# Kernel optimization log

Measured on AMD Instinct MI355X. Metric: run time of the kernel, lower is better.

## Reference

```python
import jax, jax.numpy as jnp
import numpy as np

N, E, R = 50000, 1600000, 8
IN_F, HID_F, OUT_F = 128, 64, 64


def setup_inputs() -> dict:
    key = jax.random.key(0)
    ks = jax.random.split(key, 9)
    x = jax.random.normal(ks[0], (N, IN_F), dtype=jnp.float32)
    edge_index = jax.random.randint(ks[1], (2, E), 0, N, dtype=jnp.int64)
    edge_type = jax.random.randint(ks[2], (E,), 0, R, dtype=jnp.int64)
    # layer 1 params (scaled like glorot)
    s1 = 1.0 / np.sqrt(IN_F)
    W1_rel = jax.random.normal(ks[3], (R, IN_F, HID_F), dtype=jnp.float32) * s1
    W1_root = jax.random.normal(ks[4], (IN_F, HID_F), dtype=jnp.float32) * s1
    b1 = jnp.zeros((HID_F,), dtype=jnp.float32)
    # layer 2 params
    s2 = 1.0 / np.sqrt(HID_F)
    W2_rel = jax.random.normal(ks[5], (R, HID_F, OUT_F), dtype=jnp.float32) * s2
    W2_root = jax.random.normal(ks[6], (HID_F, OUT_F), dtype=jnp.float32) * s2
    b2 = jnp.zeros((OUT_F,), dtype=jnp.float32)
    return {"x": x, "edge_index": edge_index, "edge_type": edge_type,
            "W1_rel": W1_rel, "W1_root": W1_root, "b1": b1,
            "W2_rel": W2_rel, "W2_root": W2_root, "b2": b2}


def _rgcn_conv(x, src, dst, etype, W_rel, W_root, b):
    """PyG RGCNConv: root transform + per-relation mean-aggregated messages."""
    n = x.shape[0]
    r = W_rel.shape[0]
    # per-relation transform of all node features: [R, N, H]
    xw = jnp.einsum('nd,rdh->rnh', x, W_rel)
    # per-edge message: transformed source feature under the edge's relation
    msg = xw[etype, src]  # [E, H]
    # mean normalization per (dst, relation) pair
    key = dst * r + etype  # [E]
    cnt = jax.ops.segment_sum(jnp.ones(etype.shape, dtype=x.dtype), key,
                              num_segments=n * r)
    inv = 1.0 / jnp.maximum(cnt, 1.0)
    msg = msg * inv[key][:, None]
    # scatter-add into target nodes
    agg = jax.ops.segment_sum(msg, dst, num_segments=n)  # [N, H]
    return agg + x @ W_root + b


def reference(x, edge_index, edge_type, W1_rel, W1_root, b1, W2_rel, W2_root, b2):
    src, dst = edge_index[0], edge_index[1]
    h = _rgcn_conv(x, src, dst, edge_type, W1_rel, W1_root, b1)
    h = jax.nn.relu(h)
    out = _rgcn_conv(h, src, dst, edge_type, W2_rel, W2_root, b2)
    return out
```

## Files before the change

kernel.cpp:

```cpp
#include <hip/hip_runtime.h>


constexpr int NN  = 50000;
constexpr int NE  = 1600000;
constexpr int NR  = 8;
constexpr int FIN = 128;
constexpr int FH  = 64;

constexpr int BSH = 7;
constexpr int BN  = 1 << BSH;
constexpr int NB  = (NN + BN - 1) >> BSH;
constexpr int CH  = 8192;

typedef __attribute__((ext_vector_type(8))) short bf16x8;
typedef __attribute__((ext_vector_type(4))) float f32x4;

__device__ __forceinline__ unsigned short f2bf(float f) {
  unsigned u = __float_as_uint(f);
  u = (u + 0x7fff + ((u >> 16) & 1)) >> 16;
  return (unsigned short)u;
}
__device__ __forceinline__ float bf2f(unsigned short b) {
  return __uint_as_float(((unsigned)b) << 16);
}
__device__ __forceinline__ bool edge_ok(unsigned s, unsigned d, unsigned r) {
  return s < NN && d < NN && r < NR;
}

__global__ void __launch_bounds__(256) bucket_hist(
    const int* __restrict__ src, const int* __restrict__ dst,
    const int* __restrict__ et, int* __restrict__ bhist) {
  __shared__ int h[NB];
  for (int i = threadIdx.x; i < NB; i += 256) h[i] = 0;
  __syncthreads();
  for (int i = blockIdx.x * 256 + threadIdx.x; i < NE; i += gridDim.x * 256) {
    const unsigned s = (unsigned)src[i];
    const unsigned d = (unsigned)dst[i];
    const unsigned r = (unsigned)et[i];
    if (edge_ok(s, d, r)) atomicAdd(&h[d >> BSH], 1);
  }
  __syncthreads();
  for (int i = threadIdx.x; i < NB; i += 256)
    if (h[i]) atomicAdd(&bhist[i], h[i]);
}

__global__ void __launch_bounds__(256) bucket_prefix(const int* __restrict__ bhist,
                                                     int* __restrict__ bbase,
                                                     int* __restrict__ bcur) {
  __shared__ int wtot[4];
  const int t = threadIdx.x;
  const int v0 = (2 * t < NB) ? bhist[2 * t] : 0;
  const int v1 = (2 * t + 1 < NB) ? bhist[2 * t + 1] : 0;
  const int s  = v0 + v1;
  int incl = s;
#pragma unroll
  for (int o = 1; o < 64; o <<= 1) {
    int u = __shfl_up(incl, o, 64);
    if ((t & 63) >= o) incl += u;
  }
  if ((t & 63) == 63) wtot[t >> 6] = incl;
  __syncthreads();
  int wo = 0;
  for (int w = 0; w < (t >> 6); ++w) wo += wtot[w];
  const int e = wo + incl - s;
  if (2 * t < NB)     { bbase[2 * t] = e;          bcur[2 * t] = e; }
  if (2 * t + 1 < NB) { bbase[2 * t + 1] = e + v0; bcur[2 * t + 1] = e + v0; }
}

__global__ void __launch_bounds__(256) bucket_append(
    const int* __restrict__ src, const int* __restrict__ dst,
    const int* __restrict__ et, int* __restrict__ bcur,
    uint2* __restrict__ brecs) {
  __shared__ uint2 stage[CH];
  __shared__ int h[NB], gbase[NB], sbase[NB], scur[NB];
  __shared__ int wtot[4];
  const int t  = threadIdx.x;
  const int c0 = blockIdx.x * CH;
  const int m  = min(CH, NE - c0);

  for (int i = t; i < NB; i += 256) h[i] = 0;
  __syncthreads();

  for (int i = t; i < m; i += 256) {
    const unsigned s = (unsigned)src[c0 + i];
    const unsigned d = (unsigned)dst[c0 + i];
    const unsigned r = (unsigned)et[c0 + i];
    if (edge_ok(s, d, r)) atomicAdd(&h[d >> BSH], 1);
  }
  __syncthreads();

  const int v0 = (2 * t < NB) ? h[2 * t] : 0;
  const int v1 = (2 * t + 1 < NB) ? h[2 * t + 1] : 0;
  if (2 * t < NB     && v0) gbase[2 * t]     = atomicAdd(&bcur[2 * t], v0);
  if (2 * t + 1 < NB && v1) gbase[2 * t + 1] = atomicAdd(&bcur[2 * t + 1], v1);
  const int s = v0 + v1;
  int incl = s;
#pragma unroll
  for (int o = 1; o < 64; o <<= 1) {
    int u = __shfl_up(incl, o, 64);
    if ((t & 63) >= o) incl += u;
  }
  if ((t & 63) == 63) wtot[t >> 6] = incl;
  __syncthreads();
  int wo = 0;
  for (int w = 0; w < (t >> 6); ++w) wo += wtot[w];
  const int e = wo + incl - s;
  if (2 * t < NB)     { sbase[2 * t] = e;          scur[2 * t] = e; }
  if (2 * t + 1 < NB) { sbase[2 * t + 1] = e + v0; scur[2 * t + 1] = e + v0; }
  __syncthreads();

  for (int i = t; i < m; i += 256) {
    const unsigned sv = (unsigned)src[c0 + i];
    const unsigned d  = (unsigned)dst[c0 + i];
    const unsigned r  = (unsigned)et[c0 + i];
    if (edge_ok(sv, d, r)) {
      const int p = atomicAdd(&scur[d >> BSH], 1);
      stage[p] = make_uint2((sv << 9) | (r << 6), d);
    }
  }
  __syncthreads();

  const int M = sbase[NB - 1] + h[NB - 1];
  for (int j = t; j < M; j += 256) {
    const uint2 rec = stage[j];
    const int b = (int)(rec.y >> BSH);
    brecs[gbase[b] + (j - sbase[b])] = rec;
  }
}

__global__ void __launch_bounds__(256) bucket_finalize(
    const int* __restrict__ bbase, const int* __restrict__ bhist,
    const uint2* __restrict__ brecs, float* __restrict__ inv,
    int* __restrict__ row_start, int* __restrict__ deg,
    unsigned* __restrict__ recs) {
  const int b    = blockIdx.x;
  const int base = bbase[b];
  const int m    = bhist[b];
  const int d0   = b << BSH;
  __shared__ int cnt[BN * NR];
  __shared__ int curs[BN * NR];
  __shared__ int wtot[4];
  const int t = threadIdx.x;

  for (int i = t; i < BN * NR; i += 256) cnt[i] = 0;
  __syncthreads();
  for (int i = t; i < m; i += 256) {
    const uint2 rec = brecs[base + i];
    const int dl = (int)rec.y - d0;
    const int r  = (rec.x >> 6) & 7;
    atomicAdd(&cnt[dl * NR + r], 1);
  }
  __syncthreads();

  const int c0 = cnt[t * 4], c1 = cnt[t * 4 + 1], c2 = cnt[t * 4 + 2], c3 = cnt[t * 4 + 3];
  const int s = c0 + c1 + c2 + c3;
  int incl = s;
#pragma unroll
  for (int o = 1; o < 64; o <<= 1) {
    int u = __shfl_up(incl, o, 64);
    if ((t & 63) >= o) incl += u;
  }
  if ((t & 63) == 63) wtot[t >> 6] = incl;
  __syncthreads();
  int wo = 0;
  for (int w = 0; w < (t >> 6); ++w) wo += wtot[w];
  const int e = wo + incl - s;
  curs[t * 4]     = e;
  curs[t * 4 + 1] = e + c0;
  curs[t * 4 + 2] = e + c0 + c1;
  curs[t * 4 + 3] = e + c0 + c1 + c2;
  __syncthreads();

  if (t < BN) {
    const int d = d0 + t;
    if (d < NN) {
      const int start = curs[t * NR];
      const int end   = (t == BN - 1) ? m : curs[(t + 1) * NR];
      row_start[d] = base + start;
      deg[d]       = end - start;
#pragma unroll
      for (int r = 0; r < NR; ++r)
        inv[d * NR + r] = 1.0f / fmaxf((float)cnt[t * NR + r], 1.0f);
    }
  }
  __syncthreads();

  for (int i = t; i < m; i += 256) {
    const uint2 rec = brecs[base + i];
    const int dl = (int)rec.y - d0;
    const int r  = (rec.x >> 6) & 7;
    const int p  = atomicAdd(&curs[dl * NR + r], 1);
    recs[base + p] = rec.x;
  }
}

template <int K>
__global__ void cvt_w(const float* __restrict__ Wrel, const float* __restrict__ Wroot,
                      unsigned short* __restrict__ Wt) {
  int i = blockIdx.x * blockDim.x + threadIdx.x;
  if (i >= (NR + 1) * 64 * K) return;
  const int g   = i / (64 * K);
  const int rem = i % (64 * K);
  const int n   = rem / K;
  const int k   = rem % K;
  const float* W = (g < NR) ? (Wrel + (size_t)g * K * 64) : Wroot;
  Wt[i] = f2bf(W[k * 64 + n]);
}

template <int K, bool A_FP32>
__global__ void __launch_bounds__(256) gemm_mfma(
    const void* __restrict__ Av, const unsigned short* __restrict__ Wt,
    const float* __restrict__ bias,
    unsigned short* __restrict__ xw, float* __restrict__ root_out) {
  constexpr int KP = K + 8;
  __shared__ unsigned short As[64 * KP];
  __shared__ unsigned short Bs[64 * KP];
  const int n0  = blockIdx.x * 64;
  const int tid = threadIdx.x;

  if constexpr (A_FP32) {
    const float* A = (const float*)Av;
    for (int c = tid; c < 64 * (K / 8); c += 256) {
      const int row = c / (K / 8), kp = (c % (K / 8)) * 8;
      bf16x8 v = {};
      if (n0 + row < NN) {
        const float* p = A + (size_t)(n0 + row) * K + kp;
        const float4 f0 = *(const float4*)p;
        const float4 f1 = *(const float4*)(p + 4);
        v[0] = f2bf(f0.x); v[1] = f2bf(f0.y); v[2] = f2bf(f0.z); v[3] = f2bf(f0.w);
        v[4] = f2bf(f1.x); v[5] = f2bf(f1.y); v[6] = f2bf(f1.z); v[7] = f2bf(f1.w);
      }
      *(bf16x8*)(As + row * KP + kp) = v;
    }
  } else {
    const unsigned short* A = (const unsigned short*)Av;
    for (int c = tid; c < 64 * (K / 8); c += 256) {
      const int row = c / (K / 8), kp = (c % (K / 8)) * 8;
      bf16x8 v = {};
      if (n0 + row < NN) v = *(const bf16x8*)(A + (size_t)(n0 + row) * K + kp);
      *(bf16x8*)(As + row * KP + kp) = v;
    }
  }

  const int wave = tid >> 6, lane = tid & 63;
  const int i16 = lane & 15, quad = lane >> 4;
  const int r0 = wave * 16 + i16;

  for (int g = 0; g <= NR; ++g) {
    __syncthreads();
    const unsigned short* Wg = Wt + (size_t)g * 64 * K;
    for (int c = tid; c < 64 * (K / 8); c += 256) {
      const int row = c / (K / 8), kp = (c % (K / 8)) * 8;
      *(bf16x8*)(Bs + row * KP + kp) = *(const bf16x8*)(Wg + row * K + kp);
    }
    __syncthreads();

    f32x4 acc[4] = {};
#pragma unroll
    for (int kc = 0; kc < K / 32; ++kc) {
      const int k0 = kc * 32 + quad * 8;
      const bf16x8 a0 = *(const bf16x8*)(As + r0 * KP + k0);
      const bf16x8 b0 = *(const bf16x8*)(Bs + (i16)      * KP + k0);
      const bf16x8 b1 = *(const bf16x8*)(Bs + (i16 + 16) * KP + k0);
      const bf16x8 b2 = *(const bf16x8*)(Bs + (i16 + 32) * KP + k0);
      const bf16x8 b3 = *(const bf16x8*)(Bs + (i16 + 48) * KP + k0);
      acc[0] = __builtin_amdgcn_mfma_f32_16x16x32_bf16(a0, b0, acc[0], 0, 0, 0);
      acc[1] = __builtin_amdgcn_mfma_f32_16x16x32_bf16(a0, b1, acc[1], 0, 0, 0);
      acc[2] = __builtin_amdgcn_mfma_f32_16x16x32_bf16(a0, b2, acc[2], 0, 0, 0);
      acc[3] = __builtin_amdgcn_mfma_f32_16x16x32_bf16(a0, b3, acc[3], 0, 0, 0);
    }

    if (g < NR) {
#pragma unroll
      for (int reg = 0; reg < 4; ++reg) {
        const int n = n0 + wave * 16 + quad * 4 + reg;
        if (n >= NN) continue;
        unsigned short* p = xw + (size_t)n * (NR * 64) + g * 64 + i16;
#pragma unroll
        for (int ct = 0; ct < 4; ++ct) p[ct * 16] = f2bf(acc[ct][reg]);
      }
    } else {
      float bv[4];
#pragma unroll
      for (int ct = 0; ct < 4; ++ct) bv[ct] = bias[ct * 16 + i16];
#pragma unroll
      for (int reg = 0; reg < 4; ++reg) {
        const int n = n0 + wave * 16 + quad * 4 + reg;
        if (n >= NN) continue;
        float* p = root_out + (size_t)n * 64 + i16;
#pragma unroll
        for (int ct = 0; ct < 4; ++ct) p[ct * 16] = acc[ct][reg] + bv[ct];
      }
    }
  }
}

template <bool RELU_BF16>
__global__ void __launch_bounds__(256) agg_csr(
    const int* __restrict__ row_start, const int* __restrict__ deg,
    const unsigned* __restrict__ offs, const unsigned short* __restrict__ xw,
    const float* __restrict__ inv, const float* __restrict__ root,
    float* __restrict__ out_f32, unsigned short* __restrict__ out_b16) {
  const int gid  = blockIdx.x * blockDim.x + threadIdx.x;
  const int lane = gid & 63;
  const int d    = gid >> 6;
  if (d >= NN) return;
  const int base = row_start[d];
  const int n    = deg[d];
  const float invv = inv[(d << 3) + (lane & 7)];
  float a0 = 0.f, a1 = 0.f, a2 = 0.f, a3 = 0.f;
  for (int c = 0; c < n; c += 64) {
    const int m = min(64, n - c);
    unsigned off = 0;
    if (lane < m) off = offs[base + c + lane];
    int j = 0;
    for (; j + 4 <= m; j += 4) {
      const unsigned u0 = __shfl(off, j, 64);
      const unsigned u1 = __shfl(off, j + 1, 64);
      const unsigned u2 = __shfl(off, j + 2, 64);
      const unsigned u3 = __shfl(off, j + 3, 64);
      const float s0 = __shfl(invv, (int)((u0 >> 6) & 7), 64);
      const float s1 = __shfl(invv, (int)((u1 >> 6) & 7), 64);
      const float s2 = __shfl(invv, (int)((u2 >> 6) & 7), 64);
      const float s3 = __shfl(invv, (int)((u3 >> 6) & 7), 64);
      a0 += bf2f(xw[u0 + lane]) * s0;
      a1 += bf2f(xw[u1 + lane]) * s1;
      a2 += bf2f(xw[u2 + lane]) * s2;
      a3 += bf2f(xw[u3 + lane]) * s3;
    }
    for (; j < m; ++j) {
      const unsigned u0 = __shfl(off, j, 64);
      const float s0 = __shfl(invv, (int)((u0 >> 6) & 7), 64);
      a0 += bf2f(xw[u0 + lane]) * s0;
    }
  }
  const float v = root[(size_t)d * 64 + lane] + ((a0 + a1) + (a2 + a3));
  if (RELU_BF16) out_b16[(size_t)d * 64 + lane] = f2bf(fmaxf(v, 0.f));
  else           out_f32[(size_t)d * 64 + lane] = v;
}

extern "C" void kernel_launch(void* const* d_in, const int* in_sizes, int n_in,
                              void* d_out, int out_size, void* d_ws, size_t ws_size,
                              hipStream_t stream) {
  const float* x   = (const float*)d_in[0];
  const int*   ei  = (const int*)d_in[1];
  const int*   et  = (const int*)d_in[2];
  const float* W1r = (const float*)d_in[3];
  const float* W1o = (const float*)d_in[4];
  const float* b1  = (const float*)d_in[5];
  const float* W2r = (const float*)d_in[6];
  const float* W2o = (const float*)d_in[7];
  const float* b2  = (const float*)d_in[8];
  float* out = (float*)d_out;

  const int* src = ei;
  const int* dst = ei + NE;

  char* ws = (char*)d_ws;
  size_t off = 0;
  auto alloc = [&](size_t bytes) {
    void* p = ws + off; off += (bytes + 255) & ~(size_t)255; return p;
  };
  int*   bhist     = (int*)alloc((size_t)NB * 4);
  int*   bbase     = (int*)alloc((size_t)NB * 4);
  int*   bcur      = (int*)alloc((size_t)NB * 4);
  float* inv       = (float*)alloc((size_t)NN * NR * 4);
  int*   row_start = (int*)alloc((size_t)NN * 4);
  int*   deg       = (int*)alloc((size_t)NN * 4);
  uint2* brecs     = (uint2*)alloc((size_t)NE * 8);
  unsigned* offs   = (unsigned*)alloc((size_t)NE * 4);
  unsigned short* xw    = (unsigned short*)alloc((size_t)NN * NR * 64 * 2);
  unsigned short* hb    = (unsigned short*)alloc((size_t)NN * FH * 2);
  float*          hroot = (float*)alloc((size_t)NN * 64 * 4);
  unsigned short* Wt1   = (unsigned short*)alloc((size_t)(NR + 1) * 64 * FIN * 2);
  unsigned short* Wt2   = (unsigned short*)alloc((size_t)(NR + 1) * 64 * FH * 2);

  hipMemsetAsync(bhist, 0, (size_t)NB * 4, stream);

  bucket_hist<<<256, 256, 0, stream>>>(src, dst, et, bhist);
  bucket_prefix<<<1, 256, 0, stream>>>(bhist, bbase, bcur);
  bucket_append<<<(NE + CH - 1) / CH, 256, 0, stream>>>(src, dst, et, bcur, brecs);
  bucket_finalize<<<NB, 256, 0, stream>>>(bbase, bhist, brecs, inv, row_start, deg, offs);

  cvt_w<FIN><<<((NR + 1) * 64 * FIN + 255) / 256, 256, 0, stream>>>(W1r, W1o, Wt1);
  cvt_w<FH><<<((NR + 1) * 64 * FH + 255) / 256, 256, 0, stream>>>(W2r, W2o, Wt2);

  const int gemm_blocks = (NN + 63) / 64;
  const int agg_blocks  = (NN * 64 + 255) / 256;
  gemm_mfma<FIN, true><<<gemm_blocks, 256, 0, stream>>>(x, Wt1, b1, xw, hroot);
  agg_csr<true><<<agg_blocks, 256, 0, stream>>>(row_start, deg, offs, xw, inv, hroot, nullptr, hb);
  gemm_mfma<FH, false><<<gemm_blocks, 256, 0, stream>>>(hb, Wt2, b2, xw, out);
  agg_csr<false><<<agg_blocks, 256, 0, stream>>>(row_start, deg, offs, xw, inv, out, out, nullptr);
}
```

Baseline: 292.8 us.

## Vectorize CSR aggregation to process four edges per wave with ushort4 gathers

The aggregation kernel now splits each 64-lane wave into four 16-lane groups. Each group gathers a whole 64-feature row with one 8-byte ushort4 load per lane and handles two edges per iteration, and the partial sums are combined with cross-group shuffle reductions at the end. This cuts the number of per-edge shuffles and issues wider gather loads, at the cost of tail edges being masked with zero scale and clamped offsets. The two weight-conversion kernels are also merged into one launch, and some bounds and masking hardening is added in the bucketing kernels.

```diff
diff --git a/kernel.cpp b/kernel.cpp
--- a/kernel.cpp
+++ b/kernel.cpp
@@ -11,6 +11,7 @@
 constexpr int BN  = 1 << BSH;
 constexpr int NB  = (NN + BN - 1) >> BSH;
 constexpr int CH  = 8192;
+constexpr unsigned XWMAX = (unsigned)(NN - 1) * (NR * 64) + (NR - 1) * 64;
 
 typedef __attribute__((ext_vector_type(8))) short bf16x8;
 typedef __attribute__((ext_vector_type(4))) float f32x4;
@@ -115,12 +116,12 @@
     const unsigned r  = (unsigned)et[c0 + i];
     if (edge_ok(sv, d, r)) {
       const int p = atomicAdd(&scur[d >> BSH], 1);
-      stage[p] = make_uint2((sv << 9) | (r << 6), d);
-    }
-  }
-  __syncthreads();
-
-  const int M = sbase[NB - 1] + h[NB - 1];
+      if (p < CH) stage[p] = make_uint2((sv << 9) | (r << 6), d);
+    }
+  }
+  __syncthreads();
+
+  const int M = min(sbase[NB - 1] + h[NB - 1], CH);
   for (int j = t; j < M; j += 256) {
     const uint2 rec = stage[j];
     const int b = (int)(rec.y >> BSH);
@@ -146,7 +147,7 @@
   __syncthreads();
   for (int i = t; i < m; i += 256) {
     const uint2 rec = brecs[base + i];
-    const int dl = (int)rec.y - d0;
+    const int dl = (int)(rec.y & (BN - 1));
     const int r  = (rec.x >> 6) & 7;
     atomicAdd(&cnt[dl * NR + r], 1);
   }
@@ -187,24 +188,32 @@
 
   for (int i = t; i < m; i += 256) {
     const uint2 rec = brecs[base + i];
-    const int dl = (int)rec.y - d0;
+    const int dl = (int)(rec.y & (BN - 1));
     const int r  = (rec.x >> 6) & 7;
     const int p  = atomicAdd(&curs[dl * NR + r], 1);
     recs[base + p] = rec.x;
   }
 }
 
-template <int K>
-__global__ void cvt_w(const float* __restrict__ Wrel, const float* __restrict__ Wroot,
-                      unsigned short* __restrict__ Wt) {
-  int i = blockIdx.x * blockDim.x + threadIdx.x;
-  if (i >= (NR + 1) * 64 * K) return;
-  const int g   = i / (64 * K);
-  const int rem = i % (64 * K);
-  const int n   = rem / K;
-  const int k   = rem % K;
-  const float* W = (g < NR) ? (Wrel + (size_t)g * K * 64) : Wroot;
-  Wt[i] = f2bf(W[k * 64 + n]);
+__global__ void cvt_w_all(const float* __restrict__ W1r, const float* __restrict__ W1o,
+                          const float* __restrict__ W2r, const float* __restrict__ W2o,
+                          unsigned short* __restrict__ Wt1,
+                          unsigned short* __restrict__ Wt2) {
+  const int i  = blockIdx.x * blockDim.x + threadIdx.x;
+  const int n1 = (NR + 1) * 64 * FIN;
+  const int n2 = (NR + 1) * 64 * FH;
+  if (i < n1) {
+    const int g = i / (64 * FIN), rem = i % (64 * FIN);
+    const int n = rem / FIN, k = rem % FIN;
+    const float* W = (g < NR) ? (W1r + (size_t)g * FIN * 64) : W1o;
+    Wt1[i] = f2bf(W[k * 64 + n]);
+  } else if (i < n1 + n2) {
+    const int j = i - n1;
+    const int g = j / (64 * FH), rem = j % (64 * FH);
+    const int n = rem / FH, k = rem % FH;
+    const float* W = (g < NR) ? (W2r + (size_t)g * FH * 64) : W2o;
+    Wt2[j] = f2bf(W[k * 64 + n]);
+  }
 }
 
 template <int K, bool A_FP32>
@@ -305,38 +314,52 @@
   const int lane = gid & 63;
   const int d    = gid >> 6;
   if (d >= NN) return;
+  const int e   = lane >> 4;
+  const int l16 = lane & 15;
   const int base = row_start[d];
   const int n    = deg[d];
   const float invv = inv[(d << 3) + (lane & 7)];
   float a0 = 0.f, a1 = 0.f, a2 = 0.f, a3 = 0.f;
+
   for (int c = 0; c < n; c += 64) {
     const int m = min(64, n - c);
     unsigned off = 0;
     if (lane < m) off = offs[base + c + lane];
-    int j = 0;
-    for (; j + 4 <= m; j += 4) {
-      const unsigned u0 = __shfl(off, j, 64);
-      const unsigned u1 = __shfl(off, j + 1, 64);
-      const unsigned u2 = __shfl(off, j + 2, 64);
-      const unsigned u3 = __shfl(off, j + 3, 64);
-      const float s0 = __shfl(invv, (int)((u0 >> 6) & 7), 64);
-      const float s1 = __shfl(invv, (int)((u1 >> 6) & 7), 64);
-      const float s2 = __shfl(invv, (int)((u2 >> 6) & 7), 64);
-      const float s3 = __shfl(invv, (int)((u3 >> 6) & 7), 64);
-      a0 += bf2f(xw[u0 + lane]) * s0;
-      a1 += bf2f(xw[u1 + lane]) * s1;
-      a2 += bf2f(xw[u2 + lane]) * s2;
-      a3 += bf2f(xw[u3 + lane]) * s3;
-    }
-    for (; j < m; ++j) {
-      const unsigned u0 = __shfl(off, j, 64);
-      const float s0 = __shfl(invv, (int)((u0 >> 6) & 7), 64);
-      a0 += bf2f(xw[u0 + lane]) * s0;
-    }
-  }
-  const float v = root[(size_t)d * 64 + lane] + ((a0 + a1) + (a2 + a3));
-  if (RELU_BF16) out_b16[(size_t)d * 64 + lane] = f2bf(fmaxf(v, 0.f));
-  else           out_f32[(size_t)d * 64 + lane] = v;
+    for (int j = 0; j < m; j += 8) {
+      const int i0 = j + e, i1 = j + 4 + e;
+      unsigned u0 = __shfl(off, i0 & 63, 64);
+      unsigned u1 = __shfl(off, i1 & 63, 64);
+      float s0 = __shfl(invv, (int)((u0 >> 6) & 7), 64);
+      float s1 = __shfl(invv, (int)((u1 >> 6) & 7), 64);
+      u0 = min(u0, XWMAX); u1 = min(u1, XWMAX);
+      if (i0 >= m) s0 = 0.f;
+      if (i1 >= m) s1 = 0.f;
+      const ushort4 v0 = *(const ushort4*)(xw + u0 + l16 * 4);
+      const ushort4 v1 = *(const ushort4*)(xw + u1 + l16 * 4);
+      a0 += bf2f(v0.x) * s0; a1 += bf2f(v0.y) * s0;
+      a2 += bf2f(v0.z) * s0; a3 += bf2f(v0.w) * s0;
+      a0 += bf2f(v1.x) * s1; a1 += bf2f(v1.y) * s1;
+      a2 += bf2f(v1.z) * s1; a3 += bf2f(v1.w) * s1;
+    }
+  }
+
+  a0 += __shfl_xor(a0, 16, 64); a0 += __shfl_xor(a0, 32, 64);
+  a1 += __shfl_xor(a1, 16, 64); a1 += __shfl_xor(a1, 32, 64);
+  a2 += __shfl_xor(a2, 16, 64); a2 += __shfl_xor(a2, 32, 64);
+  a3 += __shfl_xor(a3, 16, 64); a3 += __shfl_xor(a3, 32, 64);
+
+  if (e == 0) {
+    const float4 rt = *(const float4*)(root + (size_t)d * 64 + l16 * 4);
+    const float o0 = rt.x + a0, o1 = rt.y + a1, o2 = rt.z + a2, o3 = rt.w + a3;
+    if (RELU_BF16) {
+      ushort4 ov;
+      ov.x = f2bf(fmaxf(o0, 0.f)); ov.y = f2bf(fmaxf(o1, 0.f));
+      ov.z = f2bf(fmaxf(o2, 0.f)); ov.w = f2bf(fmaxf(o3, 0.f));
+      *(ushort4*)(out_b16 + (size_t)d * 64 + l16 * 4) = ov;
+    } else {
+      *(float4*)(out_f32 + (size_t)d * 64 + l16 * 4) = make_float4(o0, o1, o2, o3);
+    }
+  }
 }
 
 extern "C" void kernel_launch(void* const* d_in, const int* in_sizes, int n_in,
@@ -382,8 +405,8 @@
   bucket_append<<<(NE + CH - 1) / CH, 256, 0, stream>>>(src, dst, et, bcur, brecs);
   bucket_finalize<<<NB, 256, 0, stream>>>(bbase, bhist, brecs, inv, row_start, deg, offs);
 
-  cvt_w<FIN><<<((NR + 1) * 64 * FIN + 255) / 256, 256, 0, stream>>>(W1r, W1o, Wt1);
-  cvt_w<FH><<<((NR + 1) * 64 * FH + 255) / 256, 256, 0, stream>>>(W2r, W2o, Wt2);
+  const int ncvt = (NR + 1) * 64 * (FIN + FH);
+  cvt_w_all<<<(ncvt + 255) / 256, 256, 0, stream>>>(W1r, W1o, W2r, W2o, Wt1, Wt2);
 
   const int gemm_blocks = (NN + 63) / 64;
   const int agg_blocks  = (NN * 64 + 255) / 256;
```

Measured after the change: 278.2 us. 5.0% less time.
